# Optimization experiments

Hardware: AMD Instinct MI355X
Metric: run time of the kernel (lower is better)

The kernel has to match this reference:

```python
import jax, jax.numpy as jnp
import numpy as np

B, T, S, R, D, F = 256, 8, 200, 8, 64, 20


def setup_inputs() -> dict:
    key = jax.random.key(0)
    ks = jax.random.split(key, 8)
    # 0.1 scale keeps attention logits in a reasonable range (like trained embeddings)
    seq = 0.1 * jax.random.normal(ks[0], (B, S, D), dtype=jnp.float32)
    delta_t_n = jax.random.uniform(ks[1], (B, S), dtype=jnp.float32)  # normalized time gaps
    target = 0.1 * jax.random.normal(ks[2], (B, T, D), dtype=jnp.float32)
    target_value = 0.1 * jax.random.normal(ks[3], (B, T, R, D), dtype=jnp.float32)
    valid_mask = jax.random.randint(ks[4], (B, 1, S, 1), 0, 2, dtype=jnp.int32)
    rel_emb = 0.1 * jax.random.normal(ks[5], (R, D), dtype=jnp.float32)
    freq_real = 0.1 * jax.random.normal(ks[6], (R, F), dtype=jnp.float32)
    freq_imag = 0.1 * jax.random.normal(ks[7], (R, F), dtype=jnp.float32)
    return dict(seq=seq, delta_t_n=delta_t_n, target=target, target_value=target_value,
                valid_mask=valid_mask, rel_emb=rel_emb, freq_real=freq_real, freq_imag=freq_imag)


def _idft_decay(delta_t_n, freq_real, freq_imag):
    # freqs: concat(linspace(0,1,F)/2, -linspace(0,1,F)/2) -> [2F]
    f = jnp.linspace(0.0, 1.0, F, dtype=jnp.float32) / 2.0
    freqs = jnp.concatenate([f, -f])
    x_real = jnp.concatenate([freq_real, freq_real], axis=-1)   # [R,2F]
    x_imag = jnp.concatenate([freq_imag, -freq_imag], axis=-1)  # [R,2F]
    w = 2.0 * jnp.pi * freqs * delta_t_n[..., None]             # [B,S,2F]
    # [B,S,1,2F] * [1,1,R,2F] -> mean over 2F -> [B,S,R]
    decay = (jnp.cos(w)[:, :, None, :] * x_real[None, None]
             - jnp.sin(w)[:, :, None, :] * x_imag[None, None]).mean(axis=-1) / 2.0
    return decay


def reference(seq, delta_t_n, target, target_value, valid_mask, rel_emb, freq_real, freq_imag):
    # include_val=True branch
    rv = rel_emb[None, None] + target_value              # [B,T,R,D]
    ri = rv * target[:, :, None, :]                      # [B,T,R,D]
    # scores: contraction over D, no [B,T,S,R,D] materialization
    att = jnp.einsum('bsd,btrd->btsr', seq, ri)          # [B,T,S,R]
    att = att - att.max()
    att = jnp.where(valid_mask == 0, -jnp.inf, att)
    att = jax.nn.softmax(att, axis=-2)                   # softmax over seq (S)
    decay = jnp.clip(_idft_decay(delta_t_n, freq_real, freq_imag), 0.0, 1.0)[:, None]  # [B,1,S,R]
    decay = jnp.where(valid_mask == 0, 0.0, decay)
    att = att * decay
    context = jnp.einsum('bsd,btsr->btrd', seq, att)     # [B,T,R,D]
    return context
```

## Files before the change

### kernel.cpp

```cpp
#include <hip/hip_runtime.h>
#include <math.h>

constexpr int kB = 256, kT = 8, kS = 200, kR = 8, kD = 64, kF = 20;
constexpr int kSP = 224;
constexpr float kW1 = 3.14159265358979323846f / 19.0f;

typedef __attribute__((ext_vector_type(8))) short s16x8;
typedef __attribute__((ext_vector_type(4))) float f32x4;

__device__ __forceinline__ unsigned short bf_hi(float x, float& hf) {
    unsigned u = __float_as_uint(x) & 0xffff0000u;
    hf = __uint_as_float(u);
    return (unsigned short)(u >> 16);
}
__device__ __forceinline__ unsigned short bf_rne(float x) {
    unsigned v = __float_as_uint(x);
    return (unsigned short)((v + 0x7fffu + ((v >> 16) & 1u)) >> 16);
}

__global__ __launch_bounds__(256) void prep_kernel(
    const float* __restrict__ seq,
    const float* __restrict__ dt,
    const float* __restrict__ fr,
    const float* __restrict__ fi,
    const int*   __restrict__ vm,
    float* __restrict__ dec,
    unsigned short* __restrict__ seqH,
    unsigned short* __restrict__ seqL,
    unsigned short* __restrict__ seqTH,
    unsigned short* __restrict__ seqTL)
{
    __shared__ unsigned short lh[kS][66], ll[kS][66];

    const int b = blockIdx.x, tid = threadIdx.x;

    {
        const float4* sb = (const float4*)(seq + (size_t)b * kS * kD);
        unsigned short* gh = seqH + (size_t)b * kS * kD;
        unsigned short* gl = seqL + (size_t)b * kS * kD;
        for (int idx = tid; idx < kS * kD / 4; idx += 256) {
            float4 x = sb[idx];
            const int s = idx >> 4, d0 = (idx & 15) * 4;
            ushort4 h, lo; float hf;
            h.x = bf_hi(x.x, hf); lo.x = bf_rne(x.x - hf);
            h.y = bf_hi(x.y, hf); lo.y = bf_rne(x.y - hf);
            h.z = bf_hi(x.z, hf); lo.z = bf_rne(x.z - hf);
            h.w = bf_hi(x.w, hf); lo.w = bf_rne(x.w - hf);
            *(ushort4*)&gh[idx * 4] = h;
            *(ushort4*)&gl[idx * 4] = lo;
            *(ushort2*)&lh[s][d0]     = make_ushort2(h.x, h.y);
            *(ushort2*)&lh[s][d0 + 2] = make_ushort2(h.z, h.w);
            *(ushort2*)&ll[s][d0]     = make_ushort2(lo.x, lo.y);
            *(ushort2*)&ll[s][d0 + 2] = make_ushort2(lo.z, lo.w);
        }
    }

    {
        const int r = tid >> 5, j = tid & 31;
        float frr[kF], fir[kF];
        const float4* f4 = (const float4*)(fr + r * kF);
        const float4* g4 = (const float4*)(fi + r * kF);
#pragma unroll
        for (int c = 0; c < 5; ++c) {
            float4 a = f4[c], g = g4[c];
            frr[4*c+0]=a.x; frr[4*c+1]=a.y; frr[4*c+2]=a.z; frr[4*c+3]=a.w;
            fir[4*c+0]=g.x; fir[4*c+1]=g.y; fir[4*c+2]=g.z; fir[4*c+3]=g.w;
        }
#pragma unroll
        for (int it = 0; it < 7; ++it) {
            const int s = j + 32 * it;
            if (s < kS) {
                const float tt = dt[b * kS + s];
                const bool valid = vm[b * kS + s] != 0;
                float s1, c1;
                __sincosf(kW1 * tt, &s1, &c1);
                float ck = c1, sk = s1;
                float acc = frr[0] + c1 * frr[1] - s1 * fir[1];
#pragma unroll
                for (int k = 2; k < kF; ++k) {
                    float cn = ck * c1 - sk * s1;
                    float sn = sk * c1 + ck * s1;
                    ck = cn; sk = sn;
                    acc += ck * frr[k] - sk * fir[k];
                }
                float v = fminf(fmaxf(acc * (1.0f / (2.0f * kF)), 0.f), 1.f);
                dec[(b * kR + r) * kS + s] = valid ? v : 0.f;
            }
        }
    }
    __syncthreads();

    {
        unsigned short* th = seqTH + (size_t)b * kD * kSP;
        unsigned short* tl = seqTL + (size_t)b * kD * kSP;
        for (int idx = tid; idx < kD * kSP; idx += 256) {
            const int d = idx / kSP, s = idx - d * kSP;
            th[idx] = (s < kS) ? lh[s][d] : (unsigned short)0;
            tl[idx] = (s < kS) ? ll[s][d] : (unsigned short)0;
        }
    }
}

__global__ __launch_bounds__(256) void rda_mfma(
    const float* __restrict__ target,
    const float* __restrict__ tv,
    const int*   __restrict__ vm,
    const float* __restrict__ rel,
    const float* __restrict__ dec,
    const unsigned short* __restrict__ seqH,
    const unsigned short* __restrict__ seqL,
    const unsigned short* __restrict__ seqTH,
    const unsigned short* __restrict__ seqTL,
    float* __restrict__ out)
{
    __shared__ unsigned short riBh[16][72], riBl[16][72];
    __shared__ float attr[16][212];
    __shared__ unsigned short ath[16][232], atl[16][232];

    const int o = blockIdx.x, b = o & 255, g = o >> 8, t0 = 2 * g;
    const int tid = threadIdx.x, w = tid >> 6, l = tid & 63;
    const int lm = l & 15, lq = l >> 4;

    {
        const int n = tid >> 4, d0 = (tid & 15) * 4;
        const int tl_ = n >> 3, r = n & 7;
        const int btl = b * kT + t0 + tl_;
        float4 rv  = *(const float4*)(rel + r * kD + d0);
        float4 tvv = *(const float4*)(tv + ((size_t)btl * kR + r) * kD + d0);
        float4 tg  = *(const float4*)(target + (size_t)btl * kD + d0);
        float x[4] = {(rv.x+tvv.x)*tg.x, (rv.y+tvv.y)*tg.y,
                      (rv.z+tvv.z)*tg.z, (rv.w+tvv.w)*tg.w};
        ushort4 h, lo; float hf;
        h.x = bf_hi(x[0], hf); lo.x = bf_rne(x[0] - hf);
        h.y = bf_hi(x[1], hf); lo.y = bf_rne(x[1] - hf);
        h.z = bf_hi(x[2], hf); lo.z = bf_rne(x[2] - hf);
        h.w = bf_hi(x[3], hf); lo.w = bf_rne(x[3] - hf);
        *(ushort4*)&riBh[n][d0] = h;
        *(ushort4*)&riBl[n][d0] = lo;
    }
    __syncthreads();

    for (int Mt = w; Mt < 13; Mt += 4) {
        const int srow = min(Mt * 16 + lm, kS - 1);
        const unsigned short* ph = seqH + ((size_t)b * kS + srow) * kD;
        const unsigned short* pl = seqL + ((size_t)b * kS + srow) * kD;
        f32x4 acc = {0.f, 0.f, 0.f, 0.f};
#pragma unroll
        for (int Kt = 0; Kt < 2; ++Kt) {
            const int d0 = Kt * 32 + lq * 8;
            s16x8 ah = *(const s16x8*)&ph[d0];
            s16x8 al = *(const s16x8*)&pl[d0];
            s16x8 bh = *(const s16x8*)&riBh[lm][d0];
            s16x8 bl = *(const s16x8*)&riBl[lm][d0];
            acc = __builtin_amdgcn_mfma_f32_16x16x32_bf16(ah, bh, acc, 0, 0, 0);
            acc = __builtin_amdgcn_mfma_f32_16x16x32_bf16(ah, bl, acc, 0, 0, 0);
            acc = __builtin_amdgcn_mfma_f32_16x16x32_bf16(al, bh, acc, 0, 0, 0);
        }
        *(f32x4*)&attr[lm][Mt * 16 + lq * 4] = acc;
    }
    __syncthreads();

    {
        bool ok0 = vm[b * kS + l] != 0;
        bool ok1 = vm[b * kS + l + 64] != 0;
        bool ok2 = vm[b * kS + l + 128] != 0;
        bool ok3 = (l < 8) && (vm[b * kS + 192 + l] != 0);
        const int s3 = (l < 8) ? 192 + l : kS - 1;
#pragma unroll
        for (int j = 0; j < 4; ++j) {
            const int n = 4 * w + j, r = n & 7;
            float a0 = ok0 ? attr[n][l]       : -INFINITY;
            float a1 = ok1 ? attr[n][l + 64]  : -INFINITY;
            float a2 = ok2 ? attr[n][l + 128] : -INFINITY;
            float a3 = ok3 ? attr[n][s3]      : -INFINITY;
            float m = fmaxf(fmaxf(a0, a1), fmaxf(a2, a3));
#pragma unroll
            for (int off = 32; off; off >>= 1) m = fmaxf(m, __shfl_xor(m, off));
            float e0 = __expf(a0 - m), e1 = __expf(a1 - m);
            float e2 = __expf(a2 - m), e3 = ok3 ? __expf(a3 - m) : 0.f;
            float ssum = e0 + e1 + e2 + e3;
#pragma unroll
            for (int off = 32; off; off >>= 1) ssum += __shfl_xor(ssum, off);
            const float inv = 1.0f / ssum;
            const float* dg = dec + ((size_t)b * kR + r) * kS;
            float p0 = e0 * inv * dg[l];
            float p1 = e1 * inv * dg[l + 64];
            float p2 = e2 * inv * dg[l + 128];
            float p3 = ok3 ? e3 * inv * dg[192 + l] : 0.f;
            float hf;
            ath[n][l]       = bf_hi(p0, hf); atl[n][l]       = bf_rne(p0 - hf);
            ath[n][l + 64]  = bf_hi(p1, hf); atl[n][l + 64]  = bf_rne(p1 - hf);
            ath[n][l + 128] = bf_hi(p2, hf); atl[n][l + 128] = bf_rne(p2 - hf);
            if (l < 32) {
                float pv = (l < 8) ? p3 : 0.f;
                ath[n][192 + l] = bf_hi(pv, hf); atl[n][192 + l] = bf_rne(pv - hf);
            }
        }
    }
    __syncthreads();

    {
        const int dcol = w * 16 + lm;
        const unsigned short* th = seqTH + ((size_t)b * kD + dcol) * kSP;
        const unsigned short* tl_ = seqTL + ((size_t)b * kD + dcol) * kSP;
        f32x4 acc = {0.f, 0.f, 0.f, 0.f};
#pragma unroll
        for (int Kt = 0; Kt < 7; ++Kt) {
            const int s0 = Kt * 32 + lq * 8;
            s16x8 bh  = *(const s16x8*)&th[s0];
            s16x8 bl  = *(const s16x8*)&tl_[s0];
            s16x8 ahh = *(const s16x8*)&ath[lm][s0];
            s16x8 alo = *(const s16x8*)&atl[lm][s0];
            acc = __builtin_amdgcn_mfma_f32_16x16x32_bf16(ahh, bh, acc, 0, 0, 0);
            acc = __builtin_amdgcn_mfma_f32_16x16x32_bf16(ahh, bl, acc, 0, 0, 0);
            acc = __builtin_amdgcn_mfma_f32_16x16x32_bf16(alo, bh, acc, 0, 0, 0);
        }
#pragma unroll
        for (int i = 0; i < 4; ++i) {
            const int n = lq * 4 + i, tl2 = n >> 3, r = n & 7;
            out[(((size_t)(b * kT + t0 + tl2)) * kR + r) * kD + dcol] = acc[i];
        }
    }
}

extern "C" void kernel_launch(void* const* d_in, const int* in_sizes, int n_in,
                              void* d_out, int out_size, void* d_ws, size_t ws_size,
                              hipStream_t stream) {
    const float* seq    = (const float*)d_in[0];
    const float* dt     = (const float*)d_in[1];
    const float* target = (const float*)d_in[2];
    const float* tv     = (const float*)d_in[3];
    const int*   vm     = (const int*)  d_in[4];
    const float* rel    = (const float*)d_in[5];
    const float* fr     = (const float*)d_in[6];
    const float* fi     = (const float*)d_in[7];
    float* out = (float*)d_out;

    float* dec = (float*)d_ws;
    unsigned short* seqH  = (unsigned short*)((char*)d_ws + 1638400);
    unsigned short* seqL  = seqH + (size_t)kB * kS * kD;
    unsigned short* seqTH = seqL + (size_t)kB * kS * kD;
    unsigned short* seqTL = seqTH + (size_t)kB * kD * kSP;

    prep_kernel<<<kB, 256, 0, stream>>>(seq, dt, fr, fi, vm,
                                        dec, seqH, seqL, seqTH, seqTL);
    rda_mfma<<<kB * 4, 256, 0, stream>>>(target, tv, vm, rel, dec,
                                         seqH, seqL, seqTH, seqTL, out);
}
```

Baseline: 104.9 us.

## Split prep kernel across 32-row sequence slices for more parallel blocks

```diff
diff --git a/kernel.cpp b/kernel.cpp
--- a/kernel.cpp
+++ b/kernel.cpp
@@ -30,73 +30,80 @@
     unsigned short* __restrict__ seqTH,
     unsigned short* __restrict__ seqTL)
 {
-    __shared__ unsigned short lh[kS][66], ll[kS][66];
-
-    const int b = blockIdx.x, tid = threadIdx.x;
-
-    {
-        const float4* sb = (const float4*)(seq + (size_t)b * kS * kD);
+    __shared__ unsigned short lh[32][66], ll[32][66];
+
+    const int o = blockIdx.x, b = o & 255, slice = o >> 8;
+    const int s0 = slice * 32;
+    const int tid = threadIdx.x;
+
+    {
         unsigned short* gh = seqH + (size_t)b * kS * kD;
         unsigned short* gl = seqL + (size_t)b * kS * kD;
-        for (int idx = tid; idx < kS * kD / 4; idx += 256) {
-            float4 x = sb[idx];
-            const int s = idx >> 4, d0 = (idx & 15) * 4;
+#pragma unroll
+        for (int it = 0; it < 2; ++it) {
+            const int idx = tid + it * 256;
+            const int sl = idx >> 4, d0 = (idx & 15) * 4;
+            const int s = s0 + sl;
+            float4 x = make_float4(0.f, 0.f, 0.f, 0.f);
+            if (s < kS)
+                x = *(const float4*)(seq + ((size_t)b * kS + s) * kD + d0);
             ushort4 h, lo; float hf;
             h.x = bf_hi(x.x, hf); lo.x = bf_rne(x.x - hf);
             h.y = bf_hi(x.y, hf); lo.y = bf_rne(x.y - hf);
             h.z = bf_hi(x.z, hf); lo.z = bf_rne(x.z - hf);
             h.w = bf_hi(x.w, hf); lo.w = bf_rne(x.w - hf);
-            *(ushort4*)&gh[idx * 4] = h;
-            *(ushort4*)&gl[idx * 4] = lo;
-            *(ushort2*)&lh[s][d0]     = make_ushort2(h.x, h.y);
-            *(ushort2*)&lh[s][d0 + 2] = make_ushort2(h.z, h.w);
-            *(ushort2*)&ll[s][d0]     = make_ushort2(lo.x, lo.y);
-            *(ushort2*)&ll[s][d0 + 2] = make_ushort2(lo.z, lo.w);
-        }
-    }
-
-    {
-        const int r = tid >> 5, j = tid & 31;
-        float frr[kF], fir[kF];
-        const float4* f4 = (const float4*)(fr + r * kF);
-        const float4* g4 = (const float4*)(fi + r * kF);
-#pragma unroll
-        for (int c = 0; c < 5; ++c) {
-            float4 a = f4[c], g = g4[c];
-            frr[4*c+0]=a.x; frr[4*c+1]=a.y; frr[4*c+2]=a.z; frr[4*c+3]=a.w;
-            fir[4*c+0]=g.x; fir[4*c+1]=g.y; fir[4*c+2]=g.z; fir[4*c+3]=g.w;
-        }
-#pragma unroll
-        for (int it = 0; it < 7; ++it) {
-            const int s = j + 32 * it;
             if (s < kS) {
-                const float tt = dt[b * kS + s];
-                const bool valid = vm[b * kS + s] != 0;
-                float s1, c1;
-                __sincosf(kW1 * tt, &s1, &c1);
-                float ck = c1, sk = s1;
-                float acc = frr[0] + c1 * frr[1] - s1 * fir[1];
-#pragma unroll
-                for (int k = 2; k < kF; ++k) {
-                    float cn = ck * c1 - sk * s1;
-                    float sn = sk * c1 + ck * s1;
-                    ck = cn; sk = sn;
-                    acc += ck * frr[k] - sk * fir[k];
-                }
-                float v = fminf(fmaxf(acc * (1.0f / (2.0f * kF)), 0.f), 1.f);
-                dec[(b * kR + r) * kS + s] = valid ? v : 0.f;
-            }
-        }
-    }
-    __syncthreads();
-
-    {
-        unsigned short* th = seqTH + (size_t)b * kD * kSP;
-        unsigned short* tl = seqTL + (size_t)b * kD * kSP;
-        for (int idx = tid; idx < kD * kSP; idx += 256) {
-            const int d = idx / kSP, s = idx - d * kSP;
-            th[idx] = (s < kS) ? lh[s][d] : (unsigned short)0;
-            tl[idx] = (s < kS) ? ll[s][d] : (unsigned short)0;
+                *(ushort4*)&gh[s * kD + d0] = h;
+                *(ushort4*)&gl[s * kD + d0] = lo;
+            }
+            *(ushort2*)&lh[sl][d0]     = make_ushort2(h.x, h.y);
+            *(ushort2*)&lh[sl][d0 + 2] = make_ushort2(h.z, h.w);
+            *(ushort2*)&ll[sl][d0]     = make_ushort2(lo.x, lo.y);
+            *(ushort2*)&ll[sl][d0 + 2] = make_ushort2(lo.z, lo.w);
+        }
+    }
+
+    {
+        const int r = tid >> 5, sl = tid & 31;
+        const int s = s0 + sl;
+        if (s < kS) {
+            float frr[kF], fir[kF];
+            const float4* f4 = (const float4*)(fr + r * kF);
+            const float4* g4 = (const float4*)(fi + r * kF);
+#pragma unroll
+            for (int c = 0; c < 5; ++c) {
+                float4 a = f4[c], g = g4[c];
+                frr[4*c+0]=a.x; frr[4*c+1]=a.y; frr[4*c+2]=a.z; frr[4*c+3]=a.w;
+                fir[4*c+0]=g.x; fir[4*c+1]=g.y; fir[4*c+2]=g.z; fir[4*c+3]=g.w;
+            }
+            const float tt = dt[b * kS + s];
+            const bool valid = vm[b * kS + s] != 0;
+            float s1, c1;
+            __sincosf(kW1 * tt, &s1, &c1);
+            float ck = c1, sk = s1;
+            float acc = frr[0] + c1 * frr[1] - s1 * fir[1];
+#pragma unroll
+            for (int k = 2; k < kF; ++k) {
+                float cn = ck * c1 - sk * s1;
+                float sn = sk * c1 + ck * s1;
+                ck = cn; sk = sn;
+                acc += ck * frr[k] - sk * fir[k];
+            }
+            float v = fminf(fmaxf(acc * (1.0f / (2.0f * kF)), 0.f), 1.f);
+            dec[(b * kR + r) * kS + s] = valid ? v : 0.f;
+        }
+    }
+    __syncthreads();
+
+    {
+        unsigned short* th = seqTH + (size_t)b * kD * kSP + s0;
+        unsigned short* tl = seqTL + (size_t)b * kD * kSP + s0;
+#pragma unroll
+        for (int it = 0; it < 8; ++it) {
+            const int idx = tid + it * 256;
+            const int d = idx >> 5, sl = idx & 31;
+            th[(size_t)d * kSP + sl] = lh[sl][d];
+            tl[(size_t)d * kSP + sl] = ll[sl][d];
         }
     }
 }
@@ -242,8 +249,8 @@
     unsigned short* seqTH = seqL + (size_t)kB * kS * kD;
     unsigned short* seqTL = seqTH + (size_t)kB * kD * kSP;
 
-    prep_kernel<<<kB, 256, 0, stream>>>(seq, dt, fr, fi, vm,
-                                        dec, seqH, seqL, seqTH, seqTL);
+    prep_kernel<<<7 * kB, 256, 0, stream>>>(seq, dt, fr, fi, vm,
+                                            dec, seqH, seqL, seqTH, seqTL);
     rda_mfma<<<kB * 4, 256, 0, stream>>>(target, tv, vm, rel, dec,
                                          seqH, seqL, seqTH, seqTL, out);
 }
```

Measured after the change: 98.76 us. 1.06x faster.
